# Optimization experiments

Hardware: AMD Instinct MI355X
Metric: run time of the kernel (lower is better)

## Reference

```python
import jax, jax.numpy as jnp
import numpy as np

jax.config.update("jax_enable_x64", True)

B = 16384          # batch size (rows of features)
K = 256            # num_unlabel (clusters)
EPS = 0.05         # sinkhorn epsilon
GAMMA = 5.0        # KL regularizer weight
LR = 0.1           # SGD lr for w
MOM = 0.99         # SGD momentum
N_INNER = 3        # sinkhorn iterations
N_OUTER = 10       # outer optimization iterations


def setup_inputs() -> dict:
    key = jax.random.key(0)
    features = jax.random.normal(key, (B, K), dtype=jnp.float32)
    w = jnp.ones((1, K), dtype=jnp.float32) / K  # torch Parameter init: ones/K
    return {"features": features, "w": w, "head": 0}


def _sinkhorn(logits, w):
    """SinkhornKnopp_im.forward: logits [B,K] -> Q [B,K] (float64), preds=logits64."""
    logits64 = logits.astype(jnp.float64)
    Q = jnp.exp(logits64 / EPS).T            # [K, B]
    Q = Q / jnp.sum(Q)
    K2 = jax.nn.softmax(w, axis=1).astype(jnp.float64)  # [1, K] marginal prior
    Bn = Q.shape[1]
    for _ in range(N_INNER):
        Q = Q / jnp.sum(Q, axis=1, keepdims=True)       # row normalize
        Q = Q * K2.T                                    # scale rows by prior
        Q = Q / jnp.sum(Q, axis=0, keepdims=True)       # column normalize
        Q = Q / Bn
    Q = Q * Bn
    return Q.T, logits64                                # [B, K], [B, K]


def _total_loss(w, features):
    Q, preds = _sinkhorn(features, w)
    loss = -jnp.mean(jnp.sum(Q * preds, axis=1))
    # KLDivLoss(batchmean): input = log_softmax(w).T [K,1], target = softmax(w0).T = 1/K
    logw = jax.nn.log_softmax(w, axis=1)[0]             # [K]
    t = jnp.float32(1.0 / K)
    reg = jnp.sum(t * (jnp.log(t) - logw)) / K
    return loss + GAMMA * reg.astype(jnp.float64), Q


def reference(features, w, head):
    features = jax.lax.stop_gradient(features)  # features.detach()

    def step(carry, _):
        w, buf, _ = carry
        (_, Q), g = jax.value_and_grad(_total_loss, has_aux=True)(w, features)
        # clip_grad_norm_(params, 1)
        norm = jnp.sqrt(jnp.sum(g.astype(jnp.float64) ** 2)).astype(g.dtype)
        g = g * jnp.minimum(jnp.float32(1.0), jnp.float32(1.0) / (norm + 1e-6))
        # SGD with momentum 0.99 (buf starts at 0 -> first buf = g, matching torch)
        buf = MOM * buf + g
        w = w - LR * buf
        return (w, buf, Q), None

    Q0 = jnp.zeros((features.shape[0], K), dtype=jnp.float64)
    (w_f, buf_f, Q), _ = jax.lax.scan(
        step, (w, jnp.zeros_like(w), Q0), None, length=N_OUTER
    )
    return Q  # Q from the last outer iteration (computed with pre-update w)
```

## Files before the change

kernel.cpp:

```cpp
#include <hip/hip_runtime.h>


namespace {

constexpr int KDIM = 256;
constexpr int NBLK = 256;
constexpr int ROWS = 64;
constexpr int NRED = 16;
constexpr float L2E20 = 28.853900817779268f;

constexpr size_t P_DBL = 2ull * 256 * 512;
constexpr size_t FIN_OFF = P_DBL;
constexpr size_t FLAG_OFF_DBL = P_DBL + 4096;
constexpr int FLAG_U32 = 16384;

__device__ __forceinline__ double fast_exp_d(double x) {
  const double LOG2E  = 1.4426950408889634074;
  const double LN2_HI = 6.93147180369123816490e-01;
  const double LN2_LO = 1.90821492927058770002e-10;
  double n = rint(x * LOG2E);
  double t = fma(-n, LN2_HI, x);
  t = fma(-n, LN2_LO, t);
  double p = 2.4801587301587302e-05;
  p = fma(p, t, 1.9841269841269841e-04);
  p = fma(p, t, 1.3888888888888889e-03);
  p = fma(p, t, 8.3333333333333333e-03);
  p = fma(p, t, 4.1666666666666664e-02);
  p = fma(p, t, 1.6666666666666666e-01);
  p = fma(p, t, 0.5);
  p = fma(p, t, 1.0);
  p = fma(p, t, 1.0);
  long long ni = (long long)n;
  double s = __longlong_as_double((unsigned long long)(ni + 1023LL) << 52);
  return p * s;
}

__device__ __forceinline__ double wave_sum_d(double v) {
#pragma unroll
  for (int o = 32; o > 0; o >>= 1) v += __shfl_down(v, o);
  return v;
}
__device__ __forceinline__ double wave_max_d(double v) {
#pragma unroll
  for (int o = 32; o > 0; o >>= 1) v = fmax(v, __shfl_down(v, o));
  return v;
}

__device__ __forceinline__ double pload(const double* p) {
  return __hip_atomic_load(p, __ATOMIC_RELAXED, __HIP_MEMORY_SCOPE_AGENT);
}
__device__ __forceinline__ void pstore(double* p, double v) {
  __hip_atomic_store(p, v, __ATOMIC_RELAXED, __HIP_MEMORY_SCOPE_AGENT);
}

}

__global__ __launch_bounds__(256) void kInitWS(double* __restrict__ ws) {
  unsigned* fl = (unsigned*)(ws + FLAG_OFF_DBL);
  int idx = blockIdx.x * 256 + threadIdx.x;
  if (idx < FLAG_U32) fl[idx] = 0u;
}

__global__ __launch_bounds__(256, 1) void sink_main(
    const float* __restrict__ feat, const float* __restrict__ w_in,
    float* __restrict__ out, double* __restrict__ ws) {
  __shared__ float  Et[ROWS * KDIM];
  __shared__ float  Ft[ROWS * KDIM];
  __shared__ double alpha[KDIM];
  __shared__ double tmp1[KDIM];
  __shared__ double tmp2[KDIM];
  __shared__ double v1s[ROWS], v2s[ROWS], v3s[ROWS];
  __shared__ double grow[ROWS], wrow[ROWS], sbr[ROWS];
  __shared__ float  mrow[ROWS];
  __shared__ double sred[8];

  const int t = threadIdx.x, bid = blockIdx.x;
  const int wv = t >> 6, lane = t & 63;
  const int b0 = bid * ROWS;

  double* P = ws;
  double* fin = ws + FIN_OFF;
  unsigned* flag1 = (unsigned*)(ws + FLAG_OFF_DBL);
  unsigned* flag2 = flag1 + 8192;

  auto blk_sum = [&](double v) -> double {
    v = wave_sum_d(v);
    __syncthreads();
    if (lane == 0) sred[wv] = v;
    __syncthreads();
    return sred[0] + sred[1] + sred[2] + sred[3];
  };
  auto blk_max = [&](double v) -> double {
    v = wave_max_d(v);
    __syncthreads();
    if (lane == 0) sred[wv + 4] = v;
    __syncthreads();
    return fmax(fmax(sred[4], sred[5]), fmax(sred[6], sred[7]));
  };

  auto allreduce = [&](unsigned ph, int kind, bool pair, double pa, double pb) {
    double* row = P + (((size_t)(ph & 1)) * 256 + bid) * 512;
    pstore(&row[2 * t], pa);
    if (pair) pstore(&row[2 * t + 1], pb);
    __syncthreads();
    if (t == 0)
      __hip_atomic_store(&flag1[bid * 32], ph, __ATOMIC_RELEASE,
                         __HIP_MEMORY_SCOPE_AGENT);
    if (bid < NRED) {
      {
        const unsigned* f = &flag1[t * 32];
        while (__hip_atomic_load(f, __ATOMIC_RELAXED,
                                 __HIP_MEMORY_SCOPE_AGENT) < ph)
          __builtin_amdgcn_s_sleep(2);
      }
      __syncthreads();
      const double* base = P + ((size_t)(ph & 1)) * 131072;
      int g = t >> 4, c = t & 15;
      int k = bid * 16 + c;
      double a1 = 0.0, a2 = 0.0;
#pragma unroll
      for (int i = 0; i < 16; ++i) {
        const double* rr = base + (size_t)(g + 16 * i) * 512;
        a1 += pload(&rr[2 * k]);
        if (pair) a2 += pload(&rr[2 * k + 1]);
      }
      tmp1[t] = a1;
      if (pair) tmp2[t] = a2;
      __syncthreads();
      if (t < 16) {
        double s = 0.0;
#pragma unroll
        for (int g2 = 0; g2 < 16; ++g2) s += tmp1[g2 * 16 + t];
        pstore(&fin[(size_t)kind * 512 + (size_t)(bid * 16 + t) * 2], s);
      } else if (pair && t < 32) {
        int c2 = t - 16;
        double s = 0.0;
#pragma unroll
        for (int g2 = 0; g2 < 16; ++g2) s += tmp2[g2 * 16 + c2];
        pstore(&fin[(size_t)kind * 512 + (size_t)(bid * 16 + c2) * 2 + 1], s);
      }
      __syncthreads();
      if (t < 16)
        __hip_atomic_store(&flag2[(bid * 16 + t) * 32], ph, __ATOMIC_RELEASE,
                           __HIP_MEMORY_SCOPE_AGENT);
    }
    if (t < 16) {
      const unsigned* f = &flag2[(t * 16 + (bid & 15)) * 32];
      while (__hip_atomic_load(f, __ATOMIC_RELAXED,
                               __HIP_MEMORY_SCOPE_AGENT) < ph)
        __builtin_amdgcn_s_sleep(2);
    }
    __syncthreads();
  };

  auto row_pass = [&](double* dstv) {
    double a0 = alpha[4 * lane + 0], a1 = alpha[4 * lane + 1];
    double a2 = alpha[4 * lane + 2], a3 = alpha[4 * lane + 3];
#pragma unroll 4
    for (int r = wv; r < ROWS; r += 4) {
      float4 e4 = ((const float4*)(Et + r * KDIM))[lane];
      double s1 = a0 * (double)e4.x + a1 * (double)e4.y +
                  a2 * (double)e4.z + a3 * (double)e4.w;
      s1 = wave_sum_d(s1);
      if (lane == 0) dstv[r] = s1;
    }
  };
  auto col_partial = [&]() -> double {
    double a = 0.0;
#pragma unroll 8
    for (int r = 0; r < ROWS; ++r) a += (double)Et[r * KDIM + t] * wrow[r];
    return a;
  };

  {
    const float4* src = (const float4*)(feat + (size_t)b0 * KDIM);
    float4* dst = (float4*)Ft;
#pragma unroll
    for (int s = 0; s < 16; ++s) dst[s * 256 + t] = src[s * 256 + t];
  }
  __syncthreads();
  for (int r = wv; r < ROWS; r += 4) {
    float4 f4 = ((const float4*)(Ft + r * KDIM))[lane];
    float m = fmaxf(fmaxf(f4.x, f4.y), fmaxf(f4.z, f4.w));
#pragma unroll
    for (int o = 32; o > 0; o >>= 1) m = fmaxf(m, __shfl_down(m, o));
    if (lane == 0) {
      mrow[r] = m;
      sbr[r] = fast_exp_d(20.0 * (double)m);
    }
  }
  __syncthreads();
  double pu0 = 0.0;
#pragma unroll 8
  for (int r = 0; r < ROWS; ++r) {
    float e = exp2f((Ft[r * KDIM + t] - mrow[r]) * L2E20);
    Et[r * KDIM + t] = e;
    pu0 += (double)e * sbr[r];
  }
  float w_t = w_in[t], buf_t = 0.0f;
  double k2_t;
  {
    double x = (double)w_t;
    double m = blk_max(x);
    double e = fast_exp_d(x - m);
    double s = blk_sum(e);
    k2_t = e / s;
  }
  unsigned ph = 1;
  allreduce(ph, 0, false, pu0, 0.0);
  const double u0_t = pload(&fin[0 * 512 + 2 * t]);

  for (int it = 0; it < 10; ++it) {
    alpha[t] = k2_t / u0_t;
    __syncthreads();
    row_pass(v1s);
    __syncthreads();
    if (t < ROWS) wrow[t] = 1.0 / (16384.0 * v1s[t]);
    __syncthreads();
    {
      double pa = col_partial();
      ++ph; allreduce(ph, 1, false, pa, 0.0);
    }
    double u1_t = pload(&fin[1 * 512 + 2 * t]);

    alpha[t] = k2_t / u1_t;
    __syncthreads();
    row_pass(v2s);
    __syncthreads();
    if (t < ROWS) wrow[t] = 1.0 / (16384.0 * v2s[t]);
    __syncthreads();
    {
      double pa = col_partial();
      ++ph; allreduce(ph, 2, false, pa, 0.0);
    }
    double u2_t = pload(&fin[2 * 512 + 2 * t]);

    if (it == 9) {
      alpha[t] = k2_t / u2_t;
      __syncthreads();
      row_pass(v3s);
      __syncthreads();
      if (t < ROWS) wrow[t] = 1.0 / v3s[t];
      __syncthreads();
      double a3 = alpha[t];
#pragma unroll 4
      for (int r = 0; r < ROWS; ++r)
        out[(size_t)(b0 + r) * KDIM + t] =
            (float)(a3 * (double)Et[r * KDIM + t] * wrow[r]);
      return;
    }

    alpha[t] = k2_t / u2_t;
    __syncthreads();
    {
      double a0 = alpha[4 * lane + 0], a1 = alpha[4 * lane + 1];
      double a2 = alpha[4 * lane + 2], a3 = alpha[4 * lane + 3];
#pragma unroll 2
      for (int r = wv; r < ROWS; r += 4) {
        float4 e4 = ((const float4*)(Et + r * KDIM))[lane];
        float4 f4 = ((const float4*)(Ft + r * KDIM))[lane];
        double p0 = a0 * (double)e4.x, p1 = a1 * (double)e4.y;
        double p2 = a2 * (double)e4.z, p3 = a3 * (double)e4.w;
        double s1 = p0 + p1 + p2 + p3;
        double s2 = p0 * (double)f4.x + p1 * (double)f4.y +
                    p2 * (double)f4.z + p3 * (double)f4.w;
        s1 = wave_sum_d(s1);
        s2 = wave_sum_d(s2);
        if (lane == 0) {
          v3s[r] = s1;
          grow[r] = s2 / (16384.0 * s1 * s1);
        }
      }
    }
    __syncthreads();
    if (t < ROWS) wrow[t] = -1.0 / (16384.0 * v3s[t]);
    __syncthreads();
    {
      double ac1 = 0.0, ac2 = 0.0;
#pragma unroll 8
      for (int r = 0; r < ROWS; ++r) {
        double ed = (double)Et[r * KDIM + t];
        ac1 += ed * (double)Ft[r * KDIM + t] * wrow[r];
        ac2 += ed * grow[r];
      }
      ++ph; allreduce(ph, 3, true, ac1, ac2);
    }
    double gd_t = pload(&fin[3 * 512 + 2 * t]);
    double t3_t = pload(&fin[3 * 512 + 2 * t + 1]);

    alpha[t] = -(gd_t + t3_t) * k2_t / (u2_t * u2_t);
    __syncthreads();
    row_pass(grow);
    __syncthreads();
    if (t < ROWS) wrow[t] = -grow[t] / (16384.0 * v2s[t] * v2s[t]);
    __syncthreads();
    {
      double pa = col_partial();
      ++ph; allreduce(ph, 4, false, pa, 0.0);
    }
    double ga2_t = pload(&fin[4 * 512 + 2 * t]);

    alpha[t] = -ga2_t * k2_t / (u1_t * u1_t);
    __syncthreads();
    row_pass(grow);
    __syncthreads();
    if (t < ROWS) wrow[t] = -grow[t] / (16384.0 * v1s[t] * v1s[t]);
    __syncthreads();
    {
      double pa = col_partial();
      ++ph; allreduce(ph, 5, false, pa, 0.0);
    }
    double ga1_t = pload(&fin[5 * 512 + 2 * t]);

    {
      double gk2 = (gd_t + t3_t) / u2_t + ga2_t / u1_t + ga1_t / u0_t;
      double dot = blk_sum(k2_t * gk2);
      double gw = k2_t * (gk2 - dot) + 5.0 * (k2_t / 256.0 - 1.0 / 65536.0);
      double n2 = blk_sum(gw * gw);
      float normf = (float)sqrt(n2);
      float sc = fminf(1.0f, 1.0f / (normf + 1e-6f));
      float g = (float)gw * sc;
      buf_t = 0.99f * buf_t + g;
      w_t = w_t - 0.1f * buf_t;
      double x = (double)w_t;
      double m = blk_max(x);
      double e = fast_exp_d(x - m);
      double s = blk_sum(e);
      k2_t = e / s;
    }
  }
}

extern "C" void kernel_launch(void* const* d_in, const int* in_sizes, int n_in,
                              void* d_out, int out_size, void* d_ws,
                              size_t ws_size, hipStream_t stream) {
  (void)in_sizes; (void)n_in; (void)out_size; (void)ws_size;
  const float* feat = (const float*)d_in[0];
  const float* w_in = (const float*)d_in[1];
  float* out = (float*)d_out;
  double* ws = (double*)d_ws;

  kInitWS<<<64, 256, 0, stream>>>(ws);
  sink_main<<<NBLK, 256, 0, stream>>>(feat, w_in, out, ws);
}
```

Measured before the change: 694.3 us.

## Replace second-stage flag barrier with NaN-sentinel polling on replicated results

The grid-wide allreduce used to finish with the reducer blocks writing results and then raising a second set of flags that every block polled. Now each of the 16 reducer blocks writes its reduced values into 16 replicas, and consumers poll their own replica until it stops being NaN. Buffers are double-buffered by iteration parity, and the opposite parity is reset to NaN ahead of its next use. This removes one flag round-trip and the release ordering per allreduce. In exchange it relies on relaxed stores becoming visible without explicit release, adds more global writes for replication and NaN resets, and the sleep interval is shortened.

```diff
diff --git a/kernel.cpp b/kernel.cpp
--- a/kernel.cpp
+++ b/kernel.cpp
@@ -9,10 +9,12 @@
 constexpr int NRED = 16;
 constexpr float L2E20 = 28.853900817779268f;
 
-constexpr size_t P_DBL = 2ull * 256 * 512;
+constexpr size_t P_DBL   = 2ull * 256 * 512;
 constexpr size_t FIN_OFF = P_DBL;
-constexpr size_t FLAG_OFF_DBL = P_DBL + 4096;
-constexpr int FLAG_U32 = 16384;
+constexpr size_t FIN_PAR = 6ull * 16 * 256 * 2;
+constexpr size_t FIN_DBL = 2 * FIN_PAR;
+constexpr size_t FLAG_OFF_DBL = FIN_OFF + FIN_DBL;
+constexpr int FLAG_U32 = 256 * 32;
 
 __device__ __forceinline__ double fast_exp_d(double x) {
   const double LOG2E  = 1.4426950408889634074;
@@ -56,9 +58,13 @@
 }
 
 __global__ __launch_bounds__(256) void kInitWS(double* __restrict__ ws) {
+  const double QN = __builtin_nan("");
+  size_t gid = (size_t)blockIdx.x * 256 + threadIdx.x;
+  size_t stride = (size_t)gridDim.x * 256;
+  double* fin = ws + FIN_OFF;
+  for (size_t j = gid; j < FIN_DBL; j += stride) fin[j] = QN;
   unsigned* fl = (unsigned*)(ws + FLAG_OFF_DBL);
-  int idx = blockIdx.x * 256 + threadIdx.x;
-  if (idx < FLAG_U32) fl[idx] = 0u;
+  if (gid < FLAG_U32) fl[gid] = 0u;
 }
 
 __global__ __launch_bounds__(256, 1) void sink_main(
@@ -69,6 +75,7 @@
   __shared__ double alpha[KDIM];
   __shared__ double tmp1[KDIM];
   __shared__ double tmp2[KDIM];
+  __shared__ double sfin[32];
   __shared__ double v1s[ROWS], v2s[ROWS], v3s[ROWS];
   __shared__ double grow[ROWS], wrow[ROWS], sbr[ROWS];
   __shared__ float  mrow[ROWS];
@@ -77,11 +84,11 @@
   const int t = threadIdx.x, bid = blockIdx.x;
   const int wv = t >> 6, lane = t & 63;
   const int b0 = bid * ROWS;
+  const double QN = __builtin_nan("");
 
   double* P = ws;
   double* fin = ws + FIN_OFF;
   unsigned* flag1 = (unsigned*)(ws + FLAG_OFF_DBL);
-  unsigned* flag2 = flag1 + 8192;
 
   auto blk_sum = [&](double v) -> double {
     v = wave_sum_d(v);
@@ -98,29 +105,37 @@
     return fmax(fmax(sred[4], sred[5]), fmax(sred[6], sred[7]));
   };
 
-  auto allreduce = [&](unsigned ph, int kind, bool pair, double pa, double pb) {
+  auto allreduce = [&](unsigned ph, int kind, bool pair, int par,
+                       double pa, double pb, double& r1, double& r2) {
     double* row = P + (((size_t)(ph & 1)) * 256 + bid) * 512;
     pstore(&row[2 * t], pa);
     if (pair) pstore(&row[2 * t + 1], pb);
     __syncthreads();
     if (t == 0)
-      __hip_atomic_store(&flag1[bid * 32], ph, __ATOMIC_RELEASE,
+      __hip_atomic_store(&flag1[bid * 32], ph, __ATOMIC_RELAXED,
                          __HIP_MEMORY_SCOPE_AGENT);
     if (bid < NRED) {
+      const int rep = t >> 4, c = t & 15;
+      {
+        double* dst = fin + (size_t)(1 - par) * FIN_PAR +
+                      (size_t)kind * 8192 + (size_t)rep * 512 +
+                      2 * (size_t)(bid * 16 + c);
+        pstore(dst, QN);
+        pstore(dst + 1, QN);
+      }
       {
         const unsigned* f = &flag1[t * 32];
         while (__hip_atomic_load(f, __ATOMIC_RELAXED,
                                  __HIP_MEMORY_SCOPE_AGENT) < ph)
-          __builtin_amdgcn_s_sleep(2);
+          __builtin_amdgcn_s_sleep(1);
       }
       __syncthreads();
       const double* base = P + ((size_t)(ph & 1)) * 131072;
-      int g = t >> 4, c = t & 15;
-      int k = bid * 16 + c;
+      const int k = bid * 16 + c;
       double a1 = 0.0, a2 = 0.0;
 #pragma unroll
       for (int i = 0; i < 16; ++i) {
-        const double* rr = base + (size_t)(g + 16 * i) * 512;
+        const double* rr = base + (size_t)(rep + 16 * i) * 512;
         a1 += pload(&rr[2 * k]);
         if (pair) a2 += pload(&rr[2 * k + 1]);
       }
@@ -131,24 +146,42 @@
         double s = 0.0;
 #pragma unroll
         for (int g2 = 0; g2 < 16; ++g2) s += tmp1[g2 * 16 + t];
-        pstore(&fin[(size_t)kind * 512 + (size_t)(bid * 16 + t) * 2], s);
+        sfin[2 * t] = s;
+        if (!pair) sfin[2 * t + 1] = 0.0;
       } else if (pair && t < 32) {
         int c2 = t - 16;
         double s = 0.0;
 #pragma unroll
         for (int g2 = 0; g2 < 16; ++g2) s += tmp2[g2 * 16 + c2];
-        pstore(&fin[(size_t)kind * 512 + (size_t)(bid * 16 + c2) * 2 + 1], s);
-      }
-      __syncthreads();
-      if (t < 16)
-        __hip_atomic_store(&flag2[(bid * 16 + t) * 32], ph, __ATOMIC_RELEASE,
-                           __HIP_MEMORY_SCOPE_AGENT);
-    }
-    if (t < 16) {
-      const unsigned* f = &flag2[(t * 16 + (bid & 15)) * 32];
-      while (__hip_atomic_load(f, __ATOMIC_RELAXED,
-                               __HIP_MEMORY_SCOPE_AGENT) < ph)
-        __builtin_amdgcn_s_sleep(2);
+        sfin[2 * c2 + 1] = s;
+      }
+      __syncthreads();
+      {
+        double* dst = fin + (size_t)par * FIN_PAR + (size_t)kind * 8192 +
+                      (size_t)rep * 512 + 2 * (size_t)(bid * 16 + c);
+        pstore(dst, sfin[2 * c]);
+        if (pair) pstore(dst + 1, sfin[2 * c + 1]);
+      }
+    }
+    {
+      const double* e = fin + (size_t)par * FIN_PAR + (size_t)kind * 8192 +
+                        (size_t)(bid & 15) * 512 + 2 * (size_t)t;
+      double a;
+      for (;;) {
+        a = pload(e);
+        if (!__builtin_isnan(a)) break;
+        __builtin_amdgcn_s_sleep(1);
+      }
+      r1 = a;
+      if (pair) {
+        double b;
+        for (;;) {
+          b = pload(e + 1);
+          if (!__builtin_isnan(b)) break;
+          __builtin_amdgcn_s_sleep(1);
+        }
+        r2 = b;
+      }
     }
     __syncthreads();
   };
@@ -207,10 +240,13 @@
     k2_t = e / s;
   }
   unsigned ph = 1;
-  allreduce(ph, 0, false, pu0, 0.0);
-  const double u0_t = pload(&fin[0 * 512 + 2 * t]);
+  double u0_t, dmy;
+  allreduce(ph, 0, false, 0, pu0, 0.0, u0_t, dmy);
 
   for (int it = 0; it < 10; ++it) {
+    const int p = it & 1;
+    double u1_t, u2_t;
+
     alpha[t] = k2_t / u0_t;
     __syncthreads();
     row_pass(v1s);
@@ -219,9 +255,8 @@
     __syncthreads();
     {
       double pa = col_partial();
-      ++ph; allreduce(ph, 1, false, pa, 0.0);
-    }
-    double u1_t = pload(&fin[1 * 512 + 2 * t]);
+      ++ph; allreduce(ph, 1, false, p, pa, 0.0, u1_t, dmy);
+    }
 
     alpha[t] = k2_t / u1_t;
     __syncthreads();
@@ -231,9 +266,8 @@
     __syncthreads();
     {
       double pa = col_partial();
-      ++ph; allreduce(ph, 2, false, pa, 0.0);
-    }
-    double u2_t = pload(&fin[2 * 512 + 2 * t]);
+      ++ph; allreduce(ph, 2, false, p, pa, 0.0, u2_t, dmy);
+    }
 
     if (it == 9) {
       alpha[t] = k2_t / u2_t;
@@ -275,6 +309,7 @@
     __syncthreads();
     if (t < ROWS) wrow[t] = -1.0 / (16384.0 * v3s[t]);
     __syncthreads();
+    double gd_t, t3_t;
     {
       double ac1 = 0.0, ac2 = 0.0;
 #pragma unroll 8
@@ -283,10 +318,8 @@
         ac1 += ed * (double)Ft[r * KDIM + t] * wrow[r];
         ac2 += ed * grow[r];
       }
-      ++ph; allreduce(ph, 3, true, ac1, ac2);
-    }
-    double gd_t = pload(&fin[3 * 512 + 2 * t]);
-    double t3_t = pload(&fin[3 * 512 + 2 * t + 1]);
+      ++ph; allreduce(ph, 3, true, p, ac1, ac2, gd_t, t3_t);
+    }
 
     alpha[t] = -(gd_t + t3_t) * k2_t / (u2_t * u2_t);
     __syncthreads();
@@ -294,11 +327,11 @@
     __syncthreads();
     if (t < ROWS) wrow[t] = -grow[t] / (16384.0 * v2s[t] * v2s[t]);
     __syncthreads();
+    double ga2_t;
     {
       double pa = col_partial();
-      ++ph; allreduce(ph, 4, false, pa, 0.0);
-    }
-    double ga2_t = pload(&fin[4 * 512 + 2 * t]);
+      ++ph; allreduce(ph, 4, false, p, pa, 0.0, ga2_t, dmy);
+    }
 
     alpha[t] = -ga2_t * k2_t / (u1_t * u1_t);
     __syncthreads();
@@ -306,11 +339,11 @@
     __syncthreads();
     if (t < ROWS) wrow[t] = -grow[t] / (16384.0 * v1s[t] * v1s[t]);
     __syncthreads();
+    double ga1_t;
     {
       double pa = col_partial();
-      ++ph; allreduce(ph, 5, false, pa, 0.0);
-    }
-    double ga1_t = pload(&fin[5 * 512 + 2 * t]);
+      ++ph; allreduce(ph, 5, false, p, pa, 0.0, ga1_t, dmy);
+    }
 
     {
       double gk2 = (gd_t + t3_t) / u2_t + ga2_t / u1_t + ga1_t / u0_t;
@@ -340,6 +373,6 @@
   float* out = (float*)d_out;
   double* ws = (double*)d_ws;
 
-  kInitWS<<<64, 256, 0, stream>>>(ws);
+  kInitWS<<<128, 256, 0, stream>>>(ws);
   sink_main<<<NBLK, 256, 0, stream>>>(feat, w_in, out, ws);
 }
```

Result: faster. 558.1 us (-19.6%).
